# Optimization experiments

Measured on AMD Instinct MI355X. Metric: run time of the kernel, lower is better.

The kernel has to match this reference:

```python
import jax, jax.numpy as jnp
import numpy as np

B, S, IN_DIM = 2, 2048, 1024
DIMS, QH, KVH = 1024, 16, 4
HD = DIMS // QH          # head_dims = 64
G = QH // KVH            # groups = 4


def setup_inputs() -> dict:
    key = jax.random.key(0)
    k1, k2, k3, k4, k5, k6 = jax.random.split(key, 6)
    scale = 0.02
    q_in = jax.random.normal(k1, (B, S, IN_DIM), dtype=jnp.float32)
    kv_in = jax.random.normal(k2, (B, S, IN_DIM), dtype=jnp.float32)
    # causal mask (True = attend)
    mask = jnp.tril(jnp.ones((S, S), dtype=bool))
    Wq = jax.random.normal(k3, (IN_DIM, QH, HD), dtype=jnp.float32) * scale
    Wk = jax.random.normal(k4, (IN_DIM, KVH, HD), dtype=jnp.float32) * scale
    Wv = jax.random.normal(k5, (IN_DIM, KVH, HD), dtype=jnp.float32) * scale
    Wo = jax.random.normal(k6, (KVH * HD, IN_DIM), dtype=jnp.float32) * scale
    return {"q_in": q_in, "kv_in": kv_in, "mask": mask,
            "Wq": Wq, "Wk": Wk, "Wv": Wv, "Wo": Wo}


def reference(q_in, kv_in, mask, Wq, Wk, Wv, Wo):
    b, s, _ = q_in.shape
    # projections (DenseGeneral, no bias)
    q = jnp.einsum('bsi,ihd->bshd', q_in, Wq)   # [B,S,QH,HD]
    k = jnp.einsum('bsi,ihd->bshd', kv_in, Wk)  # [B,S,KVH,HD]
    v = jnp.einsum('bsi,ihd->bshd', kv_in, Wv)  # [B,S,KVH,HD]
    # rearrange '... s (h g) d -> ... g h s d' with g=G (h outer, g inner),
    # then einsum '... g h s d, ... h a d -> ... h s a' sums over g.
    # Equivalent (and cheaper): sum q over the group axis first.
    q_g = q.reshape(b, s, KVH, G, HD).sum(axis=3)        # [B,S,KVH,HD]
    q_g = jnp.transpose(q_g, (0, 2, 1, 3))               # [B,KVH,S,HD]
    k = jnp.transpose(k, (0, 2, 1, 3))                   # [B,KVH,S,HD]
    v = jnp.transpose(v, (0, 2, 1, 3))                   # [B,KVH,S,HD]
    scores = jnp.einsum('bhsd,bhad->bhsa', q_g, k)       # [B,KVH,S,S]
    scores = jnp.where(mask[None, None, :, :], scores, -jnp.inf)
    attn = jax.nn.softmax(scores / (HD ** 0.5), axis=-1)
    out = jnp.einsum('bhsa,bhad->bhsd', attn, v)         # [B,KVH,S,HD]
    out = jnp.transpose(out, (0, 2, 1, 3)).reshape(b, s, KVH * HD)
    return out @ Wo                                      # [B,S,IN_DIM]
```

## Files before the change

### kernel.cpp

```cpp
#include <hip/hip_runtime.h>
#include <hip/hip_bf16.h>

#define SS 2048
#define NSPLIT 8

typedef __attribute__((ext_vector_type(8))) short bf16x8;
typedef __attribute__((ext_vector_type(4))) float f32x4;

__device__ __forceinline__ short f2bf(float f){
    unsigned u = __float_as_uint(f);
    u += 0x7fff + ((u >> 16) & 1);
    return (short)(u >> 16);
}
__device__ __forceinline__ float bf2f(short s){
    return __uint_as_float(((unsigned)(unsigned short)s) << 16);
}
__device__ __forceinline__ void gload_lds16(const void* g, void* l){
    __builtin_amdgcn_global_load_lds((const __attribute__((address_space(1))) void*)g,
                                     (__attribute__((address_space(3))) void*)l, 16, 0, 0);
}

__global__ __launch_bounds__(256) void k_prep_w(const float* __restrict__ Wq,
                                                const float* __restrict__ Wk,
                                                const float* __restrict__ Wv,
                                                const float* __restrict__ Wo,
                                                const float* __restrict__ q_in,
                                                const float* __restrict__ kv_in,
                                                short* __restrict__ WcatT,
                                                short* __restrict__ WoT,
                                                short* __restrict__ Xb){
    const int bx = blockIdx.x;
    if (bx >= 256) {
        const int b2 = bx - 256;
        const float* src = (b2 < 128) ? q_in : kv_in;
        short* dst = Xb + ((b2 < 128) ? (size_t)0 : (size_t)4194304);
        const int tg = (b2 & 127) * 256 + threadIdx.x;
        #pragma unroll
        for (int j = 0; j < 8; ++j) {
            size_t off = (size_t)tg * 16 + (size_t)j * 524288;
            float4 f0 = *(const float4*)(src + off);
            float4 f1 = *(const float4*)(src + off + 4);
            float4 f2 = *(const float4*)(src + off + 8);
            float4 f3 = *(const float4*)(src + off + 12);
            short t[16];
            t[0]=f2bf(f0.x); t[1]=f2bf(f0.y); t[2]=f2bf(f0.z); t[3]=f2bf(f0.w);
            t[4]=f2bf(f1.x); t[5]=f2bf(f1.y); t[6]=f2bf(f1.z); t[7]=f2bf(f1.w);
            t[8]=f2bf(f2.x); t[9]=f2bf(f2.y); t[10]=f2bf(f2.z); t[11]=f2bf(f2.w);
            t[12]=f2bf(f3.x); t[13]=f2bf(f3.y); t[14]=f2bf(f3.z); t[15]=f2bf(f3.w);
            *(bf16x8*)(dst + off)     = *(bf16x8*)&t[0];
            *(bf16x8*)(dst + off + 8) = *(bf16x8*)&t[8];
        }
        return;
    }
    __shared__ float Ts[64][65];
    const int r  = threadIdx.x >> 2;
    const int cq = (threadIdx.x & 3) * 16;
    if (bx < 192) {
        const int ktile = bx & 15, ntile = bx >> 4;
        const int k0 = ktile * 64, n0 = ntile * 64;
        if (ntile < 4) {
            const float* base = Wq + (size_t)(k0 + r) * 1024 + ntile * 256;
            #pragma unroll
            for (int i = 0; i < 16; i += 4) {
                float4 a = *(const float4*)(base + cq + i);
                float4 b = *(const float4*)(base + 64 + cq + i);
                float4 c = *(const float4*)(base + 128 + cq + i);
                float4 d = *(const float4*)(base + 192 + cq + i);
                Ts[r][cq+i]   = 0.125f * (a.x + b.x + c.x + d.x);
                Ts[r][cq+i+1] = 0.125f * (a.y + b.y + c.y + d.y);
                Ts[r][cq+i+2] = 0.125f * (a.z + b.z + c.z + d.z);
                Ts[r][cq+i+3] = 0.125f * (a.w + b.w + c.w + d.w);
            }
        } else {
            const float* W = (ntile < 8) ? Wk : Wv;
            const float* base = W + (size_t)(k0 + r) * 256 + (ntile & 3) * 64;
            #pragma unroll
            for (int i = 0; i < 16; i += 4) {
                float4 a = *(const float4*)(base + cq + i);
                Ts[r][cq+i] = a.x; Ts[r][cq+i+1] = a.y;
                Ts[r][cq+i+2] = a.z; Ts[r][cq+i+3] = a.w;
            }
        }
        __syncthreads();
        short tmp[16];
        #pragma unroll
        for (int i = 0; i < 16; ++i) tmp[i] = f2bf(Ts[cq+i][r]);
        short* dst = WcatT + (size_t)(n0 + r) * 1024 + k0 + cq;
        *(bf16x8*)dst       = *(bf16x8*)&tmp[0];
        *(bf16x8*)(dst + 8) = *(bf16x8*)&tmp[8];
    } else {
        const int b2 = bx - 192;
        const int ktile = b2 & 3, ntile = b2 >> 2;
        const int k0 = ktile * 64, n0 = ntile * 64;
        const float* base = Wo + (size_t)(k0 + r) * 1024 + n0;
        #pragma unroll
        for (int i = 0; i < 16; i += 4) {
            float4 a = *(const float4*)(base + cq + i);
            Ts[r][cq+i] = a.x; Ts[r][cq+i+1] = a.y;
            Ts[r][cq+i+2] = a.z; Ts[r][cq+i+3] = a.w;
        }
        __syncthreads();
        short tmp[16];
        #pragma unroll
        for (int i = 0; i < 16; ++i) tmp[i] = f2bf(Ts[cq+i][r]);
        short* dst = WoT + (size_t)(n0 + r) * 256 + k0 + cq;
        *(bf16x8*)dst       = *(bf16x8*)&tmp[0];
        *(bf16x8*)(dst + 8) = *(bf16x8*)&tmp[8];
    }
}

__global__ __launch_bounds__(256) void k_gemm1(const short* __restrict__ Xb,
                                               const short* __restrict__ WcatT,
                                               short* __restrict__ pqk,
                                               short* __restrict__ vt){
    const int m0 = blockIdx.x * 64;
    const int n0 = blockIdx.y * 64;
    const short* X = Xb + ((n0 < 256) ? (size_t)0 : (size_t)4194304);
    const int tid = threadIdx.x;
    const int wave = tid >> 6, lane = tid & 63, quad = lane >> 4, l16 = lane & 15;
    const int wrow = (wave & 1) * 32, wcol = (wave >> 1) * 32;

    __shared__ char SMEM[32768];

    f32x4 acc[2][2];
    #pragma unroll
    for (int tm = 0; tm < 2; ++tm)
        #pragma unroll
        for (int tn = 0; tn < 2; ++tn) acc[tm][tn] = f32x4{0.f,0.f,0.f,0.f};

    const int lr8 = lane >> 3;
    const int sb  = ((lane & 7) * 16) ^ (lr8 << 4);
    const char* Abase = (const char*)X     + (size_t)m0 * 2048;
    const char* Bbase = (const char*)WcatT + (size_t)n0 * 2048;

    auto STAGE = [&](int buf, int k0) {
        #pragma unroll
        for (int j = 0; j < 2; ++j) {
            const int row = j * 32 + wave * 8 + lr8;
            const size_t goff = (size_t)row * 2048 + (size_t)k0 * 2 + sb;
            gload_lds16(Abase + goff, SMEM + buf * 16384 + j * 4096 + wave * 1024);
            gload_lds16(Bbase + goff, SMEM + buf * 16384 + 8192 + j * 4096 + wave * 1024);
        }
    };

    STAGE(0, 0);
    for (int k0 = 0; k0 < 1024; k0 += 64) {
        __syncthreads();
        const int cur = (k0 >> 6) & 1;
        if (k0 + 64 < 1024) STAGE(cur ^ 1, k0 + 64);
        #pragma unroll
        for (int ks = 0; ks < 2; ++ks) {
            bf16x8 a[2];
            #pragma unroll
            for (int tm = 0; tm < 2; ++tm) {
                const int R = wrow + tm * 16 + l16;
                const int cswz = ((ks * 64 + quad * 16) ^ ((R & 7) << 4));
                a[tm] = *(const bf16x8*)(SMEM + cur * 16384 + R * 128 + cswz);
            }
            #pragma unroll
            for (int tn = 0; tn < 2; ++tn) {
                const int R2 = wcol + tn * 16 + l16;
                const int cswz2 = ((ks * 64 + quad * 16) ^ ((R2 & 7) << 4));
                bf16x8 b = *(const bf16x8*)(SMEM + cur * 16384 + 8192 + R2 * 128 + cswz2);
                #pragma unroll
                for (int tm = 0; tm < 2; ++tm)
                    acc[tm][tn] = __builtin_amdgcn_mfma_f32_16x16x32_bf16(a[tm], b, acc[tm][tn], 0, 0, 0);
            }
        }
    }
    __syncthreads();

    if (n0 < 512) {
        #pragma unroll
        for (int tm = 0; tm < 2; ++tm) {
            const int mrow = m0 + wrow + tm * 16 + quad * 4;
            #pragma unroll
            for (int tn = 0; tn < 2; ++tn) {
                const int col = n0 + wcol + tn * 16 + l16;
                #pragma unroll
                for (int rg = 0; rg < 4; ++rg)
                    pqk[(size_t)(mrow + rg) * 512 + col] = f2bf(acc[tm][tn][rg]);
            }
        }
    } else {
        short* SM16 = (short*)SMEM;
        #pragma unroll
        for (int tm = 0; tm < 2; ++tm) {
            const int ml = wrow + tm * 16 + quad * 4;
            #pragma unroll
            for (int tn = 0; tn < 2; ++tn) {
                const int cl = wcol + tn * 16 + l16;
                #pragma unroll
                for (int rg = 0; rg < 4; ++rg)
                    SM16[cl * 72 + ml + rg] = f2bf(acc[tm][tn][rg]);
            }
        }
        __syncthreads();
        const int row  = tid >> 2;
        const int part = tid & 3;
        const int colv = (n0 - 512) + row;
        const int vh = colv >> 6, d = colv & 63;
        const int batch = m0 >> 11;
        const int s0 = (m0 & 2047) + part * 16;
        short* dst = vt + ((size_t)((batch * 4 + vh) * 64 + d)) * 2048 + s0;
        const short* src = &SM16[row * 72 + part * 16];
        *(bf16x8*)dst       = *(const bf16x8*)src;
        *(bf16x8*)(dst + 8) = *(const bf16x8*)(src + 8);
    }
}

__global__ __launch_bounds__(256) void k_attn4(const short* __restrict__ pqk,
                                               const short* __restrict__ vt,
                                               short* __restrict__ Op,
                                               float* __restrict__ Lp){
    const int bx = blockIdx.x;
    const int qt = 31 - (bx / NSPLIT);
    const int s  = bx - (bx / NSPLIT) * NSPLIT;
    const int kv = blockIdx.y, batch = blockIdx.z;
    const int tid = threadIdx.x;
    const int wave = tid >> 6, lane = tid & 63, quad = lane >> 4, l16 = lane & 15;
    const int r = tid >> 2, c = (tid & 3) * 16;
    const int part = (((batch * 4 + kv) * 32 + qt) * NSPLIT + s);

    __shared__ short Ks[64][72];
    __shared__ short Vs[64][72];
    __shared__ short Ps[64][72];

    const size_t qrow = (size_t)(batch * SS + qt * 64 + wave * 16 + l16);
    bf16x8 aq0 = *(const bf16x8*)(pqk + qrow * 512 + kv * 64 + quad * 8);
    bf16x8 aq1 = *(const bf16x8*)(pqk + qrow * 512 + kv * 64 + 32 + quad * 8);

    f32x4 accO[4];
    #pragma unroll
    for (int t = 0; t < 4; ++t) accO[t] = f32x4{0.f, 0.f, 0.f, 0.f};
    float lsum = 0.f;

    bf16x8 rk0, rk1, rv0, rv1;
    int kt = s;
    if (kt <= qt) {
        const short* ksrc = pqk + (size_t)(batch * SS + kt * 64 + r) * 512 + 256 + kv * 64 + c;
        rk0 = *(const bf16x8*)ksrc; rk1 = *(const bf16x8*)(ksrc + 8);
        const short* vsrc = vt + ((size_t)((batch * 4 + kv) * 64 + r)) * 2048 + kt * 64 + c;
        rv0 = *(const bf16x8*)vsrc; rv1 = *(const bf16x8*)(vsrc + 8);
    }
    for (; kt <= qt; kt += NSPLIT) {
        *(bf16x8*)&Ks[r][c]     = rk0;
        *(bf16x8*)&Ks[r][c + 8] = rk1;
        *(bf16x8*)&Vs[r][c]     = rv0;
        *(bf16x8*)&Vs[r][c + 8] = rv1;
        __syncthreads();
        if (kt + NSPLIT <= qt) {
            const short* ksrc = pqk + (size_t)(batch * SS + (kt + NSPLIT) * 64 + r) * 512 + 256 + kv * 64 + c;
            rk0 = *(const bf16x8*)ksrc; rk1 = *(const bf16x8*)(ksrc + 8);
            const short* vsrc = vt + ((size_t)((batch * 4 + kv) * 64 + r)) * 2048 + (kt + NSPLIT) * 64 + c;
            rv0 = *(const bf16x8*)vsrc; rv1 = *(const bf16x8*)(vsrc + 8);
        }

        f32x4 sc[4];
        #pragma unroll
        for (int t = 0; t < 4; ++t) sc[t] = f32x4{0.f, 0.f, 0.f, 0.f};
        #pragma unroll
        for (int ks = 0; ks < 2; ++ks) {
            bf16x8 q = ks ? aq1 : aq0;
            #pragma unroll
            for (int t = 0; t < 4; ++t) {
                bf16x8 kf = *(bf16x8*)&Ks[t * 16 + l16][ks * 32 + quad * 8];
                sc[t] = __builtin_amdgcn_mfma_f32_16x16x32_bf16(kf, q, sc[t], 0, 0, 0);
            }
        }
        if (kt == qt) {
            #pragma unroll
            for (int t = 0; t < 4; ++t) {
                #pragma unroll
                for (int rg = 0; rg < 4; ++rg)
                    if (t * 16 + quad * 4 + rg > wave * 16 + l16) sc[t][rg] = -1e30f;
            }
        }
        #pragma unroll
        for (int t = 0; t < 4; ++t) {
            float p0 = __expf(sc[t][0]);
            float p1 = __expf(sc[t][1]);
            float p2 = __expf(sc[t][2]);
            float p3 = __expf(sc[t][3]);
            lsum += (p0 + p1) + (p2 + p3);
            unsigned lo, hi;
            asm("v_cvt_pk_bf16_f32 %0, %1, %2" : "=v"(lo) : "v"(p0), "v"(p1));
            asm("v_cvt_pk_bf16_f32 %0, %1, %2" : "=v"(hi) : "v"(p2), "v"(p3));
            unsigned long long w = (unsigned long long)lo | ((unsigned long long)hi << 32);
            *(unsigned long long*)&Ps[wave * 16 + l16][t * 16 + quad * 4] = w;
        }
        #pragma unroll
        for (int ks = 0; ks < 2; ++ks) {
            bf16x8 ap = *(bf16x8*)&Ps[wave * 16 + l16][ks * 32 + quad * 8];
            #pragma unroll
            for (int t = 0; t < 4; ++t) {
                bf16x8 bv = *(bf16x8*)&Vs[t * 16 + l16][ks * 32 + quad * 8];
                accO[t] = __builtin_amdgcn_mfma_f32_16x16x32_bf16(ap, bv, accO[t], 0, 0, 0);
            }
        }
        __syncthreads();
    }
    lsum += __shfl_xor(lsum, 16);
    lsum += __shfl_xor(lsum, 32);
    #pragma unroll
    for (int rg = 0; rg < 4; ++rg) {
        int row = wave * 16 + quad * 4 + rg;
        #pragma unroll
        for (int t = 0; t < 4; ++t)
            Op[(size_t)part * 4096 + row * 64 + t * 16 + l16] = f2bf(accO[t][rg]);
    }
    if (quad == 0)
        Lp[part * 64 + wave * 16 + l16] = lsum;
}

__global__ __launch_bounds__(256) void k_combine(const short* __restrict__ Op,
                                                 const float* __restrict__ Lp,
                                                 short* __restrict__ ao){
    const int qt = blockIdx.x, kv = blockIdx.y, batch = blockIdx.z;
    const int tid = threadIdx.x;
    const int rr = tid >> 2, cs = (tid & 3) * 16;
    const int pbase = ((batch * 4 + kv) * 32 + qt) * NSPLIT;
    float lsum = 0.f;
    #pragma unroll
    for (int i = 0; i < NSPLIT; ++i) lsum += Lp[(pbase + i) * 64 + rr];
    float inv = 1.f / lsum;
    float o[16];
    #pragma unroll
    for (int j = 0; j < 16; ++j) o[j] = 0.f;
    #pragma unroll
    for (int i = 0; i < NSPLIT; ++i) {
        const short* src = Op + (size_t)(pbase + i) * 4096 + rr * 64 + cs;
        bf16x8 v0 = *(const bf16x8*)src;
        bf16x8 v1 = *(const bf16x8*)(src + 8);
        #pragma unroll
        for (int j = 0; j < 8; ++j) { o[j] += bf2f(v0[j]); o[j + 8] += bf2f(v1[j]); }
    }
    short* dst = ao + (size_t)(batch * SS + qt * 64 + rr) * 256 + kv * 64 + cs;
    #pragma unroll
    for (int j = 0; j < 16; ++j)
        dst[j] = f2bf(o[j] * inv);
}

__global__ __launch_bounds__(256) void k_gemm2(const short* __restrict__ ao,
                                               const short* __restrict__ WoT,
                                               float* __restrict__ out){
    const int m0 = blockIdx.x * 128;
    const int n0 = blockIdx.y * 128;
    const int tid = threadIdx.x;
    const int wave = tid >> 6, lane = tid & 63, quad = lane >> 4, l16 = lane & 15;
    const int wrow = (wave & 1) * 64, wcol = (wave >> 1) * 64;
    const int r = tid >> 2, cc = (tid & 3) * 16;

    __shared__ short As[128][72];
    __shared__ short Bs[128][72];

    f32x4 acc[4][4];
    #pragma unroll
    for (int tm = 0; tm < 4; ++tm)
        #pragma unroll
        for (int tn = 0; tn < 4; ++tn) acc[tm][tn] = f32x4{0.f,0.f,0.f,0.f};

    bf16x8 ra0, ra1, ra2, ra3, rb0, rb1, rb2, rb3;
    {
        const short* a0 = ao + (size_t)(m0 + r) * 256 + cc;
        const short* a1 = a0 + (size_t)64 * 256;
        const short* b0 = WoT + (size_t)(n0 + r) * 256 + cc;
        const short* b1 = b0 + (size_t)64 * 256;
        ra0 = *(const bf16x8*)a0; ra1 = *(const bf16x8*)(a0 + 8);
        ra2 = *(const bf16x8*)a1; ra3 = *(const bf16x8*)(a1 + 8);
        rb0 = *(const bf16x8*)b0; rb1 = *(const bf16x8*)(b0 + 8);
        rb2 = *(const bf16x8*)b1; rb3 = *(const bf16x8*)(b1 + 8);
    }
    for (int k0 = 0; k0 < 256; k0 += 64) {
        *(bf16x8*)&As[r][cc]          = ra0;
        *(bf16x8*)&As[r][cc + 8]      = ra1;
        *(bf16x8*)&As[r + 64][cc]     = ra2;
        *(bf16x8*)&As[r + 64][cc + 8] = ra3;
        *(bf16x8*)&Bs[r][cc]          = rb0;
        *(bf16x8*)&Bs[r][cc + 8]      = rb1;
        *(bf16x8*)&Bs[r + 64][cc]     = rb2;
        *(bf16x8*)&Bs[r + 64][cc + 8] = rb3;
        __syncthreads();
        if (k0 + 64 < 256) {
            const short* a0 = ao + (size_t)(m0 + r) * 256 + k0 + 64 + cc;
            const short* a1 = a0 + (size_t)64 * 256;
            const short* b0 = WoT + (size_t)(n0 + r) * 256 + k0 + 64 + cc;
            const short* b1 = b0 + (size_t)64 * 256;
            ra0 = *(const bf16x8*)a0; ra1 = *(const bf16x8*)(a0 + 8);
            ra2 = *(const bf16x8*)a1; ra3 = *(const bf16x8*)(a1 + 8);
            rb0 = *(const bf16x8*)b0; rb1 = *(const bf16x8*)(b0 + 8);
            rb2 = *(const bf16x8*)b1; rb3 = *(const bf16x8*)(b1 + 8);
        }
        #pragma unroll
        for (int ks = 0; ks < 2; ++ks) {
            bf16x8 a[4];
            #pragma unroll
            for (int tm = 0; tm < 4; ++tm)
                a[tm] = *(bf16x8*)&As[wrow + tm * 16 + l16][ks * 32 + quad * 8];
            #pragma unroll
            for (int tn = 0; tn < 4; ++tn) {
                bf16x8 b = *(bf16x8*)&Bs[wcol + tn * 16 + l16][ks * 32 + quad * 8];
                #pragma unroll
                for (int tm = 0; tm < 4; ++tm)
                    acc[tm][tn] = __builtin_amdgcn_mfma_f32_16x16x32_bf16(a[tm], b, acc[tm][tn], 0, 0, 0);
            }
        }
        __syncthreads();
    }
    #pragma unroll
    for (int tm = 0; tm < 4; ++tm) {
        const int mrow = m0 + wrow + tm * 16 + quad * 4;
        #pragma unroll
        for (int tn = 0; tn < 4; ++tn) {
            const int col = n0 + wcol + tn * 16 + l16;
            #pragma unroll
            for (int rg = 0; rg < 4; ++rg)
                out[(size_t)(mrow + rg) * 1024 + col] = acc[tm][tn][rg];
        }
    }
}

extern "C" void kernel_launch(void* const* d_in, const int* in_sizes, int n_in,
                              void* d_out, int out_size, void* d_ws, size_t ws_size,
                              hipStream_t stream) {
    const float* q_in  = (const float*)d_in[0];
    const float* kv_in = (const float*)d_in[1];
    int wqi = 3;
    for (int i = 2; i < n_in; ++i)
        if (in_sizes[i] == 1024 * 16 * 64) { wqi = i; break; }
    const float* Wq = (const float*)d_in[wqi];
    const float* Wk = (const float*)d_in[wqi + 1];
    const float* Wv = (const float*)d_in[wqi + 2];
    const float* Wo = (const float*)d_in[wqi + 3];
    float* out = (float*)d_out;

    char* ws = (char*)d_ws;
    short* WcatT = (short*)(ws);
    short* WoT   = (short*)(ws + 1572864);
    short* ao    = (short*)(ws + 2097152);
    short* pqk   = (short*)(ws + 4194304);
    short* vt    = (short*)(ws + 8388608);
    float* Lp    = (float*)(ws + 10485760);
    short* Op    = (short*)(ws + 33554432);
    short* Xb    = (short*)(ws + 50331648);

    hipLaunchKernelGGL(k_prep_w,  dim3(512),     dim3(256), 0, stream,
                       Wq, Wk, Wv, Wo, q_in, kv_in, WcatT, WoT, Xb);
    hipLaunchKernelGGL(k_gemm1,   dim3(64, 12),  dim3(256), 0, stream,
                       Xb, WcatT, pqk, vt);
    hipLaunchKernelGGL(k_attn4,   dim3(32 * NSPLIT, 4, 2), dim3(256), 0, stream,
                       pqk, vt, Op, Lp);
    hipLaunchKernelGGL(k_combine, dim3(32, 4, 2), dim3(256), 0, stream,
                       Op, Lp, ao);
    hipLaunchKernelGGL(k_gemm2,   dim3(32, 8),   dim3(256), 0, stream,
                       ao, WoT, out);
}
```

Before: 139.9 us.

## Fuse split-KV combine into output projection GEMM and drop combine kernel

Removes the separate k_combine kernel and the intermediate `ao` buffer. k_gemm2 now sums the per-split partial outputs and softmax denominators itself while building its A tile in LDS. This saves one launch and a write/read of the combined attention output. In exchange, every one of the 8 column blocks re-reads and re-reduces the same 8-way partial outputs, which multiplies traffic on the partial-output buffer. The register prefetch pipeline for the A/B tiles is also gone, so global loads are no longer overlapped with the MFMA work.

```diff
diff --git a/kernel.cpp b/kernel.cpp
--- a/kernel.cpp
+++ b/kernel.cpp
@@ -313,35 +313,8 @@
         Lp[part * 64 + wave * 16 + l16] = lsum;
 }
 
-__global__ __launch_bounds__(256) void k_combine(const short* __restrict__ Op,
-                                                 const float* __restrict__ Lp,
-                                                 short* __restrict__ ao){
-    const int qt = blockIdx.x, kv = blockIdx.y, batch = blockIdx.z;
-    const int tid = threadIdx.x;
-    const int rr = tid >> 2, cs = (tid & 3) * 16;
-    const int pbase = ((batch * 4 + kv) * 32 + qt) * NSPLIT;
-    float lsum = 0.f;
-    #pragma unroll
-    for (int i = 0; i < NSPLIT; ++i) lsum += Lp[(pbase + i) * 64 + rr];
-    float inv = 1.f / lsum;
-    float o[16];
-    #pragma unroll
-    for (int j = 0; j < 16; ++j) o[j] = 0.f;
-    #pragma unroll
-    for (int i = 0; i < NSPLIT; ++i) {
-        const short* src = Op + (size_t)(pbase + i) * 4096 + rr * 64 + cs;
-        bf16x8 v0 = *(const bf16x8*)src;
-        bf16x8 v1 = *(const bf16x8*)(src + 8);
-        #pragma unroll
-        for (int j = 0; j < 8; ++j) { o[j] += bf2f(v0[j]); o[j + 8] += bf2f(v1[j]); }
-    }
-    short* dst = ao + (size_t)(batch * SS + qt * 64 + rr) * 256 + kv * 64 + cs;
-    #pragma unroll
-    for (int j = 0; j < 16; ++j)
-        dst[j] = f2bf(o[j] * inv);
-}
-
-__global__ __launch_bounds__(256) void k_gemm2(const short* __restrict__ ao,
+__global__ __launch_bounds__(256) void k_gemm2(const short* __restrict__ Op,
+                                               const float* __restrict__ Lp,
                                                const short* __restrict__ WoT,
                                                float* __restrict__ out){
     const int m0 = blockIdx.x * 128;
@@ -350,9 +323,24 @@
     const int wave = tid >> 6, lane = tid & 63, quad = lane >> 4, l16 = lane & 15;
     const int wrow = (wave & 1) * 64, wcol = (wave >> 1) * 64;
     const int r = tid >> 2, cc = (tid & 3) * 16;
+    const int batch = m0 >> 11;
+    const int qt0 = (m0 & 2047) >> 6;
 
     __shared__ short As[128][72];
     __shared__ short Bs[128][72];
+    __shared__ float invLs[512];
+
+    #pragma unroll
+    for (int h = 0; h < 2; ++h) {
+        const int v = tid + h * 256;
+        const int kvv = v >> 7, r0 = v & 127;
+        const int qt = qt0 + (r0 >> 6), rin = r0 & 63;
+        const int pb = ((batch * 4 + kvv) * 32 + qt) * NSPLIT;
+        float ls = 0.f;
+        #pragma unroll
+        for (int i = 0; i < NSPLIT; ++i) ls += Lp[(pb + i) * 64 + rin];
+        invLs[v] = 1.f / ls;
+    }
 
     f32x4 acc[4][4];
     #pragma unroll
@@ -360,37 +348,50 @@
         #pragma unroll
         for (int tn = 0; tn < 4; ++tn) acc[tm][tn] = f32x4{0.f,0.f,0.f,0.f};
 
-    bf16x8 ra0, ra1, ra2, ra3, rb0, rb1, rb2, rb3;
-    {
-        const short* a0 = ao + (size_t)(m0 + r) * 256 + cc;
-        const short* a1 = a0 + (size_t)64 * 256;
-        const short* b0 = WoT + (size_t)(n0 + r) * 256 + cc;
-        const short* b1 = b0 + (size_t)64 * 256;
-        ra0 = *(const bf16x8*)a0; ra1 = *(const bf16x8*)(a0 + 8);
-        ra2 = *(const bf16x8*)a1; ra3 = *(const bf16x8*)(a1 + 8);
-        rb0 = *(const bf16x8*)b0; rb1 = *(const bf16x8*)(b0 + 8);
-        rb2 = *(const bf16x8*)b1; rb3 = *(const bf16x8*)(b1 + 8);
-    }
+    __syncthreads();
+
     for (int k0 = 0; k0 < 256; k0 += 64) {
-        *(bf16x8*)&As[r][cc]          = ra0;
-        *(bf16x8*)&As[r][cc + 8]      = ra1;
-        *(bf16x8*)&As[r + 64][cc]     = ra2;
-        *(bf16x8*)&As[r + 64][cc + 8] = ra3;
-        *(bf16x8*)&Bs[r][cc]          = rb0;
-        *(bf16x8*)&Bs[r][cc + 8]      = rb1;
-        *(bf16x8*)&Bs[r + 64][cc]     = rb2;
-        *(bf16x8*)&Bs[r + 64][cc + 8] = rb3;
-        __syncthreads();
-        if (k0 + 64 < 256) {
-            const short* a0 = ao + (size_t)(m0 + r) * 256 + k0 + 64 + cc;
-            const short* a1 = a0 + (size_t)64 * 256;
-            const short* b0 = WoT + (size_t)(n0 + r) * 256 + k0 + 64 + cc;
+        const int kv = k0 >> 6;
+        const int pbA = ((batch * 4 + kv) * 32 + qt0) * NSPLIT;
+        const int pbB = pbA + NSPLIT;
+        float o0[16], o1[16];
+        #pragma unroll
+        for (int j = 0; j < 16; ++j) { o0[j] = 0.f; o1[j] = 0.f; }
+        #pragma unroll
+        for (int i = 0; i < NSPLIT; ++i) {
+            const short* sA = Op + (size_t)(pbA + i) * 4096 + r * 64 + cc;
+            bf16x8 a0 = *(const bf16x8*)sA;
+            bf16x8 a1 = *(const bf16x8*)(sA + 8);
+            const short* sB = Op + (size_t)(pbB + i) * 4096 + r * 64 + cc;
+            bf16x8 b0 = *(const bf16x8*)sB;
+            bf16x8 b1 = *(const bf16x8*)(sB + 8);
+            #pragma unroll
+            for (int j = 0; j < 8; ++j) {
+                o0[j] += bf2f(a0[j]); o0[j + 8] += bf2f(a1[j]);
+                o1[j] += bf2f(b0[j]); o1[j + 8] += bf2f(b1[j]);
+            }
+        }
+        const float i0 = invLs[kv * 128 + r];
+        const float i1 = invLs[kv * 128 + 64 + r];
+        short t0[16], t1[16];
+        #pragma unroll
+        for (int j = 0; j < 16; ++j) {
+            t0[j] = f2bf(o0[j] * i0);
+            t1[j] = f2bf(o1[j] * i1);
+        }
+        *(bf16x8*)&As[r][cc]          = *(bf16x8*)&t0[0];
+        *(bf16x8*)&As[r][cc + 8]      = *(bf16x8*)&t0[8];
+        *(bf16x8*)&As[r + 64][cc]     = *(bf16x8*)&t1[0];
+        *(bf16x8*)&As[r + 64][cc + 8] = *(bf16x8*)&t1[8];
+        {
+            const short* b0 = WoT + (size_t)(n0 + r) * 256 + k0 + cc;
             const short* b1 = b0 + (size_t)64 * 256;
-            ra0 = *(const bf16x8*)a0; ra1 = *(const bf16x8*)(a0 + 8);
-            ra2 = *(const bf16x8*)a1; ra3 = *(const bf16x8*)(a1 + 8);
-            rb0 = *(const bf16x8*)b0; rb1 = *(const bf16x8*)(b0 + 8);
-            rb2 = *(const bf16x8*)b1; rb3 = *(const bf16x8*)(b1 + 8);
-        }
+            *(bf16x8*)&Bs[r][cc]          = *(const bf16x8*)b0;
+            *(bf16x8*)&Bs[r][cc + 8]      = *(const bf16x8*)(b0 + 8);
+            *(bf16x8*)&Bs[r + 64][cc]     = *(const bf16x8*)b1;
+            *(bf16x8*)&Bs[r + 64][cc + 8] = *(const bf16x8*)(b1 + 8);
+        }
+        __syncthreads();
         #pragma unroll
         for (int ks = 0; ks < 2; ++ks) {
             bf16x8 a[4];
@@ -437,7 +438,6 @@
     char* ws = (char*)d_ws;
     short* WcatT = (short*)(ws);
     short* WoT   = (short*)(ws + 1572864);
-    short* ao    = (short*)(ws + 2097152);
     short* pqk   = (short*)(ws + 4194304);
     short* vt    = (short*)(ws + 8388608);
     float* Lp    = (float*)(ws + 10485760);
@@ -450,8 +450,6 @@
                        Xb, WcatT, pqk, vt);
     hipLaunchKernelGGL(k_attn4,   dim3(32 * NSPLIT, 4, 2), dim3(256), 0, stream,
                        pqk, vt, Op, Lp);
-    hipLaunchKernelGGL(k_combine, dim3(32, 4, 2), dim3(256), 0, stream,
-                       Op, Lp, ao);
     hipLaunchKernelGGL(k_gemm2,   dim3(32, 8),   dim3(256), 0, stream,
-                       ao, WoT, out);
-}
+                       Op, Lp, WoT, out);
+}
```

Result: slower. 147.6 us (+5.5%).
